# Optimization experiments

Hardware: AMD Instinct MI355X
Metric: run time of the kernel (lower is better)

Reference implementation:

```python
import jax, jax.numpy as jnp
import numpy as np

N_NODES = 50000
N_EDGES = 800000
H = 128          # hidden_channels
R = 20           # num_radial
L = 3            # num_layers
CUTOFF = 5.0
N_ATOM_TYPE = 100


def setup_inputs() -> dict:
    key = jax.random.key(0)
    ks = jax.random.split(key, 24)
    z = jax.random.randint(ks[0], (N_NODES,), 0, N_ATOM_TYPE)
    edge_index = jax.random.randint(ks[1], (2, N_EDGES), 0, N_NODES)
    # distances in (0.05, cutoff] so the 1/d term in the RBF stays bounded
    edge_dist = 0.05 + jax.random.uniform(ks[2], (N_EDGES,), jnp.float32) * (CUTOFF - 0.05)
    edge_vec = jax.random.normal(ks[3], (N_EDGES, 3), jnp.float32)
    s = 0.05
    emb = jax.random.normal(ks[4], (N_ATOM_TYPE, H), jnp.float32) * s
    # stacked per-layer params, torch Linear stored as [in, out]
    msg_w1 = jax.random.normal(ks[5], (L, H, H), jnp.float32) * s
    msg_b1 = jnp.zeros((L, H), jnp.float32)
    msg_w2 = jax.random.normal(ks[6], (L, H, 3 * H), jnp.float32) * s
    msg_b2 = jnp.zeros((L, 3 * H), jnp.float32)
    rbf_w = jax.random.normal(ks[7], (L, R, 3 * H), jnp.float32) * s
    rbf_b = jnp.zeros((L, 3 * H), jnp.float32)
    upd_vw = jax.random.normal(ks[8], (L, H, 2 * H), jnp.float32) * s
    upd_w1 = jax.random.normal(ks[9], (L, 2 * H, H), jnp.float32) * s
    upd_b1 = jnp.zeros((L, H), jnp.float32)
    upd_w2 = jax.random.normal(ks[10], (L, H, 3 * H), jnp.float32) * s
    upd_b2 = jnp.zeros((L, 3 * H), jnp.float32)
    out_w1 = jax.random.normal(ks[11], (H, H // 2), jnp.float32) * s
    out_b1 = jnp.zeros((H // 2,), jnp.float32)
    out_w2 = jax.random.normal(ks[12], (H // 2, 1), jnp.float32) * s
    out_b2 = jnp.zeros((1,), jnp.float32)
    return {
        "z": z, "edge_index": edge_index, "edge_dist": edge_dist, "edge_vec": edge_vec,
        "emb": emb,
        "msg_w1": msg_w1, "msg_b1": msg_b1, "msg_w2": msg_w2, "msg_b2": msg_b2,
        "rbf_w": rbf_w, "rbf_b": rbf_b,
        "upd_vw": upd_vw, "upd_w1": upd_w1, "upd_b1": upd_b1,
        "upd_w2": upd_w2, "upd_b2": upd_b2,
        "out_w1": out_w1, "out_b1": out_b1, "out_w2": out_w2, "out_b2": out_b2,
    }


def reference(z, edge_index, edge_dist, edge_vec, emb,
              msg_w1, msg_b1, msg_w2, msg_b2, rbf_w, rbf_b,
              upd_vw, upd_w1, upd_b1, upd_w2, upd_b2,
              out_w1, out_b1, out_w2, out_b2):
    inv_sqrt3 = 1.0 / float(np.sqrt(3.0))
    inv_sqrtH = 1.0 / float(np.sqrt(H))
    inv_sqrt2 = 1.0 / float(np.sqrt(2.0))

    src, dst = edge_index[0], edge_index[1]
    n_nodes = z.shape[0]

    # unit edge direction vectors
    unit = edge_vec / jnp.linalg.norm(edge_vec, axis=-1, keepdims=True)

    # radial basis (RadialBasisLayer)
    d = edge_dist[:, None]                                   # [E,1]
    cosc = 0.5 * (jnp.cos(jnp.pi * edge_dist / CUTOFF) + 1.0)
    cosc = jnp.where(edge_dist <= CUTOFF, cosc, 0.0)         # [E]
    n_idx = jnp.arange(1, R + 1, dtype=edge_dist.dtype)       # [R]
    rbf = (jnp.sin(n_idx * jnp.pi * d / CUTOFF) / d) * cosc[:, None]  # [E,R]

    s = emb[z]                                                # [N,H]
    v = jnp.zeros((n_nodes, 3, H), s.dtype)                   # [N,3,H]

    for l in range(L):
        # --- MessageBlock ---
        mf = jax.nn.silu(s @ msg_w1[l] + msg_b1[l]) @ msg_w2[l] + msg_b2[l]  # [N,3H]
        wf = rbf @ rbf_w[l] + rbf_b[l]                                       # [E,3H]
        prod = mf[src] * wf                                                  # [E,3H]
        w_s, w_vs, w_vv = jnp.split(prod, 3, axis=-1)                        # [E,H] x3
        w_v = v[src] * w_vs[:, None, :] * inv_sqrt3 + w_vv[:, None, :] * unit[:, :, None]  # [E,3,H]
        ds = jax.ops.segment_sum(w_s, dst, num_segments=n_nodes)             # [N,H]
        dv = jax.ops.segment_sum(w_v, dst, num_segments=n_nodes) * inv_sqrtH # [N,3,H]
        s = s + ds
        v = v + dv

        # --- UpdateBlock ---
        vv = v @ upd_vw[l]                                                   # [N,3,2H]
        v1, v2 = jnp.split(vv, 2, axis=-1)                                   # [N,3,H] x2
        v_dot = jnp.einsum('nij,nij->nj', v1, v2) * inv_sqrtH                # [N,H]
        v_norm = jnp.sqrt(jnp.sum(v2 * v2, axis=1) + 1e-12)                  # [N,H]
        feat = jnp.concatenate([s, v_norm], axis=-1)                         # [N,2H]
        uf = jax.nn.silu(feat @ upd_w1[l] + upd_b1[l]) @ upd_w2[l] + upd_b2[l]  # [N,3H]
        a_ss, a_sv, a_v = jnp.split(uf, 3, axis=-1)
        s = s + (v_dot * a_sv + a_ss) * inv_sqrt2
        v = v + v1 * a_v[:, None, :]

    # output MLP + mean readout
    h = jax.nn.silu(s @ out_w1 + out_b1) @ out_w2 + out_b2                   # [N,1]
    return jnp.mean(h, axis=0)                                               # [1]
```

## Files before the change

### kernel.cpp

```cpp
#include <hip/hip_runtime.h>
#include <hip/hip_bf16.h>
#include <math.h>

__device__ __forceinline__ float silu_f(float x) { return x / (1.0f + expf(-x)); }

__global__ __launch_bounds__(256) void k_init_s(const int* __restrict__ z,
                                                const float* __restrict__ emb,
                                                float* __restrict__ s, int total4) {
    int idx = blockIdx.x * 256 + threadIdx.x;
    if (idx < total4) {
        int n = idx >> 5, c4 = idx & 31;
        ((float4*)s)[idx] = ((const float4*)emb)[(size_t)z[n] * 32 + c4];
    }
}

__global__ __launch_bounds__(256) void k_count(const int* __restrict__ ei, int* __restrict__ cnt,
                                               int nE) {
    int e = blockIdx.x * 256 + threadIdx.x;
    if (e < nE) atomicAdd(&cnt[ei[nE + e]], 1);
}

__global__ __launch_bounds__(1024) void k_scan_blk(const int* __restrict__ cnt,
                                                   int* __restrict__ offs,
                                                   int* __restrict__ btot, int N) {
    __shared__ int tmp[1024];
    const int tid = threadIdx.x;
    int i = blockIdx.x * 1024 + tid;
    int val = (i < N) ? cnt[i] : 0;
    tmp[tid] = val;
    __syncthreads();
    for (int off = 1; off < 1024; off <<= 1) {
        int t = (tid >= off) ? tmp[tid - off] : 0;
        __syncthreads();
        tmp[tid] += t;
        __syncthreads();
    }
    if (i < N) offs[i] = tmp[tid] - val;
    if (tid == 1023) btot[blockIdx.x] = tmp[1023];
}

__global__ void k_scan_top(const int* __restrict__ btot, int* __restrict__ btot2,
                           int nb, int* __restrict__ offsN) {
    int tid = threadIdx.x;
    int v = (tid < nb) ? btot[tid] : 0;
    int orig = v;
    #pragma unroll
    for (int off = 1; off < 64; off <<= 1) {
        int u = __shfl_up(v, off, 64);
        if (tid >= off) v += u;
    }
    btot2[tid] = v - orig;
    if (tid == 63) *offsN = v;
}

__global__ __launch_bounds__(256) void k_scan_add(int* __restrict__ offs,
                                                  const int* __restrict__ btot2, int N) {
    int i = blockIdx.x * 256 + threadIdx.x;
    if (i < N) offs[i] += btot2[i >> 10];
}

__global__ __launch_bounds__(256) void k_fill(const int* __restrict__ ei,
                                              const int* __restrict__ offs,
                                              int* __restrict__ cur, int* __restrict__ perm,
                                              int nE) {
    int e = blockIdx.x * 256 + threadIdx.x;
    if (e < nE) {
        int d = ei[nE + e];
        int p = atomicAdd(&cur[d], 1);
        perm[offs[d] + p] = e;
    }
}

__global__ __launch_bounds__(256) void k_prep(const float* __restrict__ edist,
                                              int* __restrict__ perm,
                                              float2* __restrict__ curc2,
                                              int nE, int nEpad) {
    int i = blockIdx.x * 256 + threadIdx.x;
    if (i >= nEpad) return;
    if (i >= nE) { perm[i] = 0; curc2[i] = make_float2(0.f, 0.f); return; }
    int e = perm[i];
    float dd = edist[e];
    float t = 0.62831853071795864769f * dd;
    float cs = cosf(t), sn = sinf(t);
    float cosc = (dd <= 5.0f) ? (0.5f * (cs + 1.0f)) : 0.0f;
    float ic = cosc / dd;
    curc2[i] = make_float2(sn * ic, 2.0f * cs);
}

__global__ __launch_bounds__(256, 4) void k_mf(const float* __restrict__ s,
                                               const float* __restrict__ W1,
                                               const float* __restrict__ b1,
                                               const float* __restrict__ W2,
                                               const float* __restrict__ b2,
                                               float* __restrict__ mf) {
    __shared__ float s_t[16 * 128];
    __shared__ float h_t[16 * 128];
    const int tid = threadIdx.x;
    const size_t nb = (size_t)blockIdx.x * 16;
    {
        const float4* p = (const float4*)(s + nb * 128);
        ((float4*)s_t)[tid] = p[tid];
        ((float4*)s_t)[tid + 256] = p[tid + 256];
    }
    __syncthreads();
    const int c = tid & 127;
    const int g = tid >> 7;
    {
        float acc[8];
        float bb = b1[c];
        #pragma unroll
        for (int i = 0; i < 8; i++) acc[i] = bb;
        for (int k = 0; k < 128; k += 4) {
            float4 sv[8];
            #pragma unroll
            for (int i = 0; i < 8; i++) sv[i] = *(const float4*)&s_t[(g * 8 + i) * 128 + k];
            #pragma unroll
            for (int kk = 0; kk < 4; kk++) {
                float w = W1[(size_t)(k + kk) * 128 + c];
                #pragma unroll
                for (int i = 0; i < 8; i++) acc[i] = fmaf((&sv[i].x)[kk], w, acc[i]);
            }
        }
        #pragma unroll
        for (int i = 0; i < 8; i++) h_t[(g * 8 + i) * 128 + c] = silu_f(acc[i]);
    }
    __syncthreads();
    {
        float acc[8][3];
        #pragma unroll
        for (int q = 0; q < 3; q++) {
            float bb = b2[c + 128 * q];
            #pragma unroll
            for (int i = 0; i < 8; i++) acc[i][q] = bb;
        }
        for (int k = 0; k < 128; k += 4) {
            float4 hv[8];
            #pragma unroll
            for (int i = 0; i < 8; i++) hv[i] = *(const float4*)&h_t[(g * 8 + i) * 128 + k];
            #pragma unroll
            for (int kk = 0; kk < 4; kk++) {
                float w0 = W2[(size_t)(k + kk) * 384 + c];
                float w1 = W2[(size_t)(k + kk) * 384 + c + 128];
                float w2 = W2[(size_t)(k + kk) * 384 + c + 256];
                #pragma unroll
                for (int i = 0; i < 8; i++) {
                    float a = (&hv[i].x)[kk];
                    acc[i][0] = fmaf(a, w0, acc[i][0]);
                    acc[i][1] = fmaf(a, w1, acc[i][1]);
                    acc[i][2] = fmaf(a, w2, acc[i][2]);
                }
            }
        }
        #pragma unroll
        for (int i = 0; i < 8; i++)
            #pragma unroll
            for (int q = 0; q < 3; q++)
                mf[(nb + g * 8 + i) * 384 + c + 128 * q] = acc[i][q];
    }
}

__global__ __launch_bounds__(256, 2) void k_edge3(const int* __restrict__ ei,
                                                  const float* __restrict__ evec,
                                                  const float* __restrict__ mf,
                                                  const float* __restrict__ v,
                                                  const float* __restrict__ Wr,
                                                  const float* __restrict__ br,
                                                  const int* __restrict__ offs,
                                                  const int* __restrict__ perm,
                                                  const float2* __restrict__ curc2,
                                                  float* __restrict__ s,
                                                  float* __restrict__ dV,
                                                  int nN) {
    __shared__ float wrl[8064];
    for (int t = threadIdx.x; t < 8064; t += 256)
        wrl[t] = (t < 7680) ? Wr[t] : br[t - 7680];
    __syncthreads();

    const int lane = threadIdx.x & 63;
    const int wvi = __builtin_amdgcn_readfirstlane(threadIdx.x >> 6);
    const int nbase = blockIdx.x * 16 + wvi * 4;
    const float inv_sqrt3 = 0.57735026918962576451f;

    float brv[6];
    #pragma unroll
    for (int q = 0; q < 6; ++q) brv[q] = wrl[7680 + q * 64 + lane];

    for (int j = 0; j < 4; ++j) {
        const int n = nbase + j;
        if (n >= nN) break;
        const int beg = offs[n], end = offs[n + 1];

        float sa0 = 0.f, sa1 = 0.f;
        float dv00 = 0.f, dv10 = 0.f, dv20 = 0.f;
        float dv01 = 0.f, dv11 = 0.f, dv21 = 0.f;

        for (int i = beg; i < end; i += 4) {
            const int ne = end - i;
            int src[4];
            float ux[4], uy[4], uz[4], cur[4], prev[4], c2v[4];
            #pragma unroll
            for (int t = 0; t < 4; ++t) {
                int e = perm[i + t];
                float2 cc = curc2[i + t];
                cur[t] = cc.x; c2v[t] = cc.y; prev[t] = 0.f;
                src[t] = ei[e];
                float ex = evec[3 * e], ey = evec[3 * e + 1], ez = evec[3 * e + 2];
                float rn = 1.0f / sqrtf(ex * ex + ey * ey + ez * ez);
                ux[t] = ex * rn; uy[t] = ey * rn; uz[t] = ez * rn;
            }
            float wf[4][6];
            #pragma unroll
            for (int t = 0; t < 4; ++t)
                #pragma unroll
                for (int q = 0; q < 6; ++q) wf[t][q] = brv[q];
            for (int rr = 0; rr < 20; ++rr) {
                float w6[6];
                #pragma unroll
                for (int q = 0; q < 6; ++q) w6[q] = wrl[rr * 384 + q * 64 + lane];
                #pragma unroll
                for (int t = 0; t < 4; ++t) {
                    float c = cur[t];
                    #pragma unroll
                    for (int q = 0; q < 6; ++q) wf[t][q] = fmaf(c, w6[q], wf[t][q]);
                    float nx = fmaf(c2v[t], c, -prev[t]);
                    prev[t] = c; cur[t] = nx;
                }
            }
            #pragma unroll
            for (int t = 0; t < 4; ++t) {
                if (t < ne) {
                    const float* mfr = mf + (size_t)src[t] * 384 + lane;
                    const float* vr  = v  + (size_t)src[t] * 384 + lane;
                    sa0 = fmaf(wf[t][0], mfr[0],  sa0);
                    sa1 = fmaf(wf[t][1], mfr[64], sa1);
                    float a0 = wf[t][2] * mfr[128] * inv_sqrt3;
                    float a1 = wf[t][3] * mfr[192] * inv_sqrt3;
                    float b0 = wf[t][4] * mfr[256];
                    float b1 = wf[t][5] * mfr[320];
                    dv00 = fmaf(vr[0],   a0, fmaf(ux[t], b0, dv00));
                    dv10 = fmaf(vr[128], a0, fmaf(uy[t], b0, dv10));
                    dv20 = fmaf(vr[256], a0, fmaf(uz[t], b0, dv20));
                    dv01 = fmaf(vr[64],  a1, fmaf(ux[t], b1, dv01));
                    dv11 = fmaf(vr[192], a1, fmaf(uy[t], b1, dv11));
                    dv21 = fmaf(vr[320], a1, fmaf(uz[t], b1, dv21));
                }
            }
        }
        float* sp = s + (size_t)n * 128;
        sp[lane] += sa0;
        sp[64 + lane] += sa1;
        float* dp = dV + (size_t)n * 384;
        dp[lane] = dv00;        dp[64 + lane] = dv01;
        dp[128 + lane] = dv10;  dp[192 + lane] = dv11;
        dp[256 + lane] = dv20;  dp[320 + lane] = dv21;
    }
}

__global__ __launch_bounds__(256, 4) void k_upd(float* __restrict__ s,
                                                float* __restrict__ v,
                                                const float* __restrict__ dV,
                                                const float* __restrict__ Wv,
                                                const float* __restrict__ W1,
                                                const float* __restrict__ b1,
                                                const float* __restrict__ W2,
                                                const float* __restrict__ b2) {
    __shared__ float sv[8 * 128];
    __shared__ float vn[8 * 384];
    __shared__ float vnl[8 * 128];
    __shared__ float u1[8 * 128];
    const int tid = threadIdx.x;
    const size_t nb = (size_t)blockIdx.x * 8;
    const float inv_sqrtH = 0.08838834764831845f;
    const float inv_sqrt2 = 0.70710678118654752440f;

    {
        ((float4*)sv)[tid] = ((const float4*)(s + nb * 128))[tid];
        const float4* v4 = (const float4*)(v + nb * 384);
        const float4* e4 = (const float4*)(dV + nb * 384);
        #pragma unroll
        for (int t = 0; t < 3; ++t) {
            float4 av = v4[tid + 256 * t], bv = e4[tid + 256 * t];
            ((float4*)vn)[tid + 256 * t] =
                make_float4(fmaf(bv.x, inv_sqrtH, av.x), fmaf(bv.y, inv_sqrtH, av.y),
                            fmaf(bv.z, inv_sqrtH, av.z), fmaf(bv.w, inv_sqrtH, av.w));
        }
    }
    __syncthreads();
    const int c0 = tid & 63;
    const int ty = tid >> 6;
    float acc[2][3][4];
    {
        #pragma unroll
        for (int i = 0; i < 2; i++)
            #pragma unroll
            for (int d = 0; d < 3; d++)
                #pragma unroll
                for (int cc = 0; cc < 4; cc++) acc[i][d][cc] = 0.f;
        for (int k = 0; k < 128; k += 4) {
            float4 av[2][3];
            #pragma unroll
            for (int i = 0; i < 2; i++)
                #pragma unroll
                for (int d = 0; d < 3; d++)
                    av[i][d] = *(const float4*)&vn[(ty * 2 + i) * 384 + d * 128 + k];
            #pragma unroll
            for (int kk = 0; kk < 4; kk++) {
                float wc[4];
                #pragma unroll
                for (int cc = 0; cc < 4; cc++) wc[cc] = Wv[(size_t)(k + kk) * 256 + c0 + 64 * cc];
                #pragma unroll
                for (int i = 0; i < 2; i++)
                    #pragma unroll
                    for (int d = 0; d < 3; d++) {
                        float a = (&av[i][d].x)[kk];
                        #pragma unroll
                        for (int cc = 0; cc < 4; cc++)
                            acc[i][d][cc] = fmaf(a, wc[cc], acc[i][d][cc]);
                    }
            }
        }
    }
    float vdot[2][2];
    {
        #pragma unroll
        for (int i = 0; i < 2; i++)
            #pragma unroll
            for (int hh = 0; hh < 2; hh++) {
                float d0 = acc[i][0][hh] * acc[i][0][hh + 2] + acc[i][1][hh] * acc[i][1][hh + 2] +
                           acc[i][2][hh] * acc[i][2][hh + 2];
                vdot[i][hh] = d0 * inv_sqrtH;
                float n2 = acc[i][0][hh + 2] * acc[i][0][hh + 2] +
                           acc[i][1][hh + 2] * acc[i][1][hh + 2] +
                           acc[i][2][hh + 2] * acc[i][2][hh + 2];
                vnl[(ty * 2 + i) * 128 + c0 + 64 * hh] = sqrtf(n2 + 1e-12f);
            }
    }
    __syncthreads();
    {
        float a3[2][2];
        float bb0 = b1[c0], bb1 = b1[c0 + 64];
        #pragma unroll
        for (int i = 0; i < 2; i++) { a3[i][0] = bb0; a3[i][1] = bb1; }
        for (int k = 0; k < 128; k += 4) {
            float4 f[2];
            #pragma unroll
            for (int i = 0; i < 2; i++) f[i] = *(const float4*)&sv[(ty * 2 + i) * 128 + k];
            #pragma unroll
            for (int kk = 0; kk < 4; kk++) {
                float w0 = W1[(size_t)(k + kk) * 128 + c0];
                float w1 = W1[(size_t)(k + kk) * 128 + c0 + 64];
                #pragma unroll
                for (int i = 0; i < 2; i++) {
                    float a = (&f[i].x)[kk];
                    a3[i][0] = fmaf(a, w0, a3[i][0]);
                    a3[i][1] = fmaf(a, w1, a3[i][1]);
                }
            }
        }
        for (int k = 0; k < 128; k += 4) {
            float4 f[2];
            #pragma unroll
            for (int i = 0; i < 2; i++) f[i] = *(const float4*)&vnl[(ty * 2 + i) * 128 + k];
            #pragma unroll
            for (int kk = 0; kk < 4; kk++) {
                float w0 = W1[(size_t)(k + kk + 128) * 128 + c0];
                float w1 = W1[(size_t)(k + kk + 128) * 128 + c0 + 64];
                #pragma unroll
                for (int i = 0; i < 2; i++) {
                    float a = (&f[i].x)[kk];
                    a3[i][0] = fmaf(a, w0, a3[i][0]);
                    a3[i][1] = fmaf(a, w1, a3[i][1]);
                }
            }
        }
        #pragma unroll
        for (int i = 0; i < 2; i++) {
            u1[(ty * 2 + i) * 128 + c0] = silu_f(a3[i][0]);
            u1[(ty * 2 + i) * 128 + c0 + 64] = silu_f(a3[i][1]);
        }
    }
    __syncthreads();
    {
        float a4[2][6];
        #pragma unroll
        for (int q = 0; q < 6; q++) {
            float bb = b2[c0 + 64 * q];
            #pragma unroll
            for (int i = 0; i < 2; i++) a4[i][q] = bb;
        }
        for (int k = 0; k < 128; k += 4) {
            float4 uu[2];
            #pragma unroll
            for (int i = 0; i < 2; i++) uu[i] = *(const float4*)&u1[(ty * 2 + i) * 128 + k];
            #pragma unroll
            for (int kk = 0; kk < 4; kk++) {
                float w[6];
                #pragma unroll
                for (int q = 0; q < 6; q++) w[q] = W2[(size_t)(k + kk) * 384 + c0 + 64 * q];
                #pragma unroll
                for (int i = 0; i < 2; i++) {
                    float a = (&uu[i].x)[kk];
                    #pragma unroll
                    for (int q = 0; q < 6; q++) a4[i][q] = fmaf(a, w[q], a4[i][q]);
                }
            }
        }
        #pragma unroll
        for (int i = 0; i < 2; i++) {
            int node = ty * 2 + i;
            size_t nr = nb + node;
            #pragma unroll
            for (int hh = 0; hh < 2; ++hh) {
                int h = c0 + 64 * hh;
                float a_ss = a4[i][hh], a_sv = a4[i][2 + hh], a_v = a4[i][4 + hh];
                s[nr * 128 + h] = sv[node * 128 + h] + (vdot[i][hh] * a_sv + a_ss) * inv_sqrt2;
                #pragma unroll
                for (int d = 0; d < 3; ++d)
                    v[nr * 384 + d * 128 + h] =
                        vn[node * 384 + d * 128 + h] + acc[i][d][hh] * a_v;
            }
        }
    }
}

__global__ __launch_bounds__(256, 4) void k_out(const float* __restrict__ s,
                                                const float* __restrict__ ow1,
                                                const float* __restrict__ ob1,
                                                const float* __restrict__ ow2,
                                                const float* __restrict__ ob2,
                                                float* __restrict__ out, int nNodes) {
    __shared__ float st[16 * 128];
    __shared__ float red[4];
    const int tid = threadIdx.x;
    const size_t nb = (size_t)blockIdx.x * 16;
    {
        const float4* p = (const float4*)(s + nb * 128);
        ((float4*)st)[tid] = p[tid];
        ((float4*)st)[tid + 256] = p[tid + 256];
    }
    __syncthreads();
    const int c = tid & 63;
    const int ty = tid >> 6;
    float acc[4];
    float bb = ob1[c];
    #pragma unroll
    for (int i = 0; i < 4; i++) acc[i] = bb;
    for (int k = 0; k < 128; k += 4) {
        float4 sv[4];
        #pragma unroll
        for (int i = 0; i < 4; i++) sv[i] = *(const float4*)&st[(ty * 4 + i) * 128 + k];
        #pragma unroll
        for (int kk = 0; kk < 4; kk++) {
            float w = ow1[(size_t)(k + kk) * 64 + c];
            #pragma unroll
            for (int i = 0; i < 4; i++) acc[i] = fmaf((&sv[i].x)[kk], w, acc[i]);
        }
    }
    float w2 = ow2[c];
    float p = 0.f;
    #pragma unroll
    for (int i = 0; i < 4; i++) p += silu_f(acc[i]) * w2;
    #pragma unroll
    for (int off = 32; off > 0; off >>= 1) p += __shfl_down(p, off, 64);
    if (c == 0) red[ty] = p;
    __syncthreads();
    if (tid == 0) {
        float val = (red[0] + red[1] + red[2] + red[3]) * (1.0f / (float)nNodes);
        if (blockIdx.x == 0) val += ob2[0];
        atomicAdd(out, val);
    }
}

extern "C" void kernel_launch(void* const* d_in, const int* in_sizes, int n_in,
                              void* d_out, int out_size, void* d_ws, size_t ws_size,
                              hipStream_t stream) {
    const int*   z     = (const int*)d_in[0];
    const int*   ei    = (const int*)d_in[1];
    const float* edist = (const float*)d_in[2];
    const float* evec  = (const float*)d_in[3];
    const float* emb   = (const float*)d_in[4];
    const float* mw1   = (const float*)d_in[5];
    const float* mb1   = (const float*)d_in[6];
    const float* mw2   = (const float*)d_in[7];
    const float* mb2   = (const float*)d_in[8];
    const float* rw    = (const float*)d_in[9];
    const float* rbb   = (const float*)d_in[10];
    const float* uvw   = (const float*)d_in[11];
    const float* uw1   = (const float*)d_in[12];
    const float* ub1   = (const float*)d_in[13];
    const float* uw2   = (const float*)d_in[14];
    const float* ub2   = (const float*)d_in[15];
    const float* ow1   = (const float*)d_in[16];
    const float* ob1   = (const float*)d_in[17];
    const float* ow2   = (const float*)d_in[18];
    const float* ob2   = (const float*)d_in[19];

    const int N = in_sizes[0];
    const int E = in_sizes[2];
    const int Ep = E + 4;

    const size_t need = ((size_t)N * 1280 + (N + 1) + Ep) * 4 + (size_t)Ep * 8;
    hipMemsetAsync(d_out, 0, out_size * sizeof(float), stream);
    if (ws_size < need) return;

    float* ws = (float*)d_ws;
    float*  s     = ws;
    float*  v     = s + (size_t)N * 128;
    float*  mf    = v + (size_t)N * 384;
    float*  dV    = mf + (size_t)N * 384;
    int*    offs  = (int*)(dV + (size_t)N * 384);
    int*    perm  = offs + (N + 1);
    float2* curc2 = (float2*)(perm + Ep);
    int*    cnt   = (int*)curc2;
    int*    cur   = cnt + N;
    int*    btot  = cur + N;
    int*    btot2 = btot + 64;

    hipMemsetAsync(v, 0, (size_t)N * 384 * sizeof(float), stream);
    hipMemsetAsync(cnt, 0, (size_t)2 * N * sizeof(int), stream);

    const int nbScan = (N + 1023) / 1024;
    k_count<<<(E + 255) / 256, 256, 0, stream>>>(ei, cnt, E);
    k_scan_blk<<<nbScan, 1024, 0, stream>>>(cnt, offs, btot, N);
    k_scan_top<<<1, 64, 0, stream>>>(btot, btot2, nbScan, offs + N);
    k_scan_add<<<(N + 255) / 256, 256, 0, stream>>>(offs, btot2, N);
    k_fill<<<(E + 255) / 256, 256, 0, stream>>>(ei, offs, cur, perm, E);
    k_prep<<<(Ep + 255) / 256, 256, 0, stream>>>(edist, perm, curc2, E, Ep);

    k_init_s<<<(N * 32 + 255) / 256, 256, 0, stream>>>(z, emb, s, N * 32);

    for (int l = 0; l < 3; ++l) {
        k_mf<<<N / 16, 256, 0, stream>>>(s, mw1 + (size_t)l * 16384, mb1 + l * 128,
                                         mw2 + (size_t)l * 49152, mb2 + l * 384, mf);
        k_edge3<<<(N + 15) / 16, 256, 0, stream>>>(ei, evec, mf, v,
                                                   rw + (size_t)l * 7680, rbb + l * 384,
                                                   offs, perm, curc2, s, dV, N);
        k_upd<<<N / 8, 256, 0, stream>>>(s, v, dV, uvw + (size_t)l * 32768,
                                         uw1 + (size_t)l * 32768, ub1 + l * 128,
                                         uw2 + (size_t)l * 49152, ub2 + l * 384);
    }
    k_out<<<N / 16, 256, 0, stream>>>(s, ow1, ob1, ow2, ob2, (float*)d_out, N);
}
```

Baseline: 3.193 ms.

## Software-pipeline edge gathers and double node tile in update kernel

The edge kernel now double-buffers per-edge metadata (perm, source index, unit vector, Chebyshev state) using A/B register sets. It also issues the mf and v gathers for the current group of four edges before the radial-basis FMA loop, so gather latency overlaps with compute. The update kernel processes 16 nodes per block instead of 8, which doubles reuse of each weight load from global memory, and its occupancy hint drops from 4 to 3. The costs are much higher register pressure in both kernels, possible spills, and lower occupancy. The padded perm/curc2 arrays are assumed to cover the prefetch tail.

Result: slower. 9.546 ms (+199.0%).

```diff
diff --git a/kernel.cpp b/kernel.cpp
--- a/kernel.cpp
+++ b/kernel.cpp
@@ -159,7 +159,68 @@
     }
 }
 
-__global__ __launch_bounds__(256, 2) void k_edge3(const int* __restrict__ ei,
+#define LOAD_META(SUF, II)                                                     \
+    _Pragma("unroll")                                                          \
+    for (int t = 0; t < 4; ++t) {                                              \
+        int e = perm[(II) + t];                                                \
+        float2 cc = curc2[(II) + t];                                           \
+        cur##SUF[t] = cc.x; c2##SUF[t] = cc.y; prev##SUF[t] = 0.f;             \
+        src##SUF[t] = ei[e];                                                   \
+        float ex = evec[3 * e], ey = evec[3 * e + 1], ez = evec[3 * e + 2];    \
+        float rn = 1.0f / sqrtf(ex * ex + ey * ey + ez * ez);                  \
+        ux##SUF[t] = ex * rn; uy##SUF[t] = ey * rn; uz##SUF[t] = ez * rn;      \
+    }
+
+#define PROC(CUR, OTH)                                                         \
+    {                                                                          \
+        float gm[4][6], gv[4][6];                                              \
+        _Pragma("unroll")                                                      \
+        for (int t = 0; t < 4; ++t) {                                          \
+            const float* mfr = mf + (size_t)src##CUR[t] * 384 + lane;          \
+            const float* vr  = v  + (size_t)src##CUR[t] * 384 + lane;          \
+            _Pragma("unroll")                                                  \
+            for (int q = 0; q < 6; ++q) { gm[t][q] = mfr[q * 64]; gv[t][q] = vr[q * 64]; } \
+        }                                                                      \
+        if (i + 4 < end) { LOAD_META(OTH, i + 4) }                             \
+        float wf[4][6];                                                        \
+        _Pragma("unroll")                                                      \
+        for (int t = 0; t < 4; ++t)                                            \
+            _Pragma("unroll")                                                  \
+            for (int q = 0; q < 6; ++q) wf[t][q] = brv[q];                     \
+        for (int rr = 0; rr < 20; ++rr) {                                      \
+            float w6[6];                                                       \
+            _Pragma("unroll")                                                  \
+            for (int q = 0; q < 6; ++q) w6[q] = wrl[rr * 384 + q * 64 + lane]; \
+            _Pragma("unroll")                                                  \
+            for (int t = 0; t < 4; ++t) {                                      \
+                float c = cur##CUR[t];                                         \
+                _Pragma("unroll")                                              \
+                for (int q = 0; q < 6; ++q) wf[t][q] = fmaf(c, w6[q], wf[t][q]); \
+                float nx = fmaf(c2##CUR[t], c, -prev##CUR[t]);                 \
+                prev##CUR[t] = c; cur##CUR[t] = nx;                            \
+            }                                                                  \
+        }                                                                      \
+        const int ne = end - i;                                                \
+        _Pragma("unroll")                                                      \
+        for (int t = 0; t < 4; ++t) {                                          \
+            if (t < ne) {                                                      \
+                sa0 = fmaf(wf[t][0], gm[t][0], sa0);                           \
+                sa1 = fmaf(wf[t][1], gm[t][1], sa1);                           \
+                float a0 = wf[t][2] * gm[t][2] * inv_sqrt3;                    \
+                float a1 = wf[t][3] * gm[t][3] * inv_sqrt3;                    \
+                float b0 = wf[t][4] * gm[t][4];                                \
+                float b1 = wf[t][5] * gm[t][5];                                \
+                dv00 = fmaf(gv[t][0], a0, fmaf(ux##CUR[t], b0, dv00));         \
+                dv10 = fmaf(gv[t][2], a0, fmaf(uy##CUR[t], b0, dv10));         \
+                dv20 = fmaf(gv[t][4], a0, fmaf(uz##CUR[t], b0, dv20));         \
+                dv01 = fmaf(gv[t][1], a1, fmaf(ux##CUR[t], b1, dv01));         \
+                dv11 = fmaf(gv[t][3], a1, fmaf(uy##CUR[t], b1, dv11));         \
+                dv21 = fmaf(gv[t][5], a1, fmaf(uz##CUR[t], b1, dv21));         \
+            }                                                                  \
+        }                                                                      \
+    }
+
+__global__ __launch_bounds__(256, 2) void k_edge4(const int* __restrict__ ei,
                                                   const float* __restrict__ evec,
                                                   const float* __restrict__ mf,
                                                   const float* __restrict__ v,
@@ -194,58 +255,20 @@
         float dv00 = 0.f, dv10 = 0.f, dv20 = 0.f;
         float dv01 = 0.f, dv11 = 0.f, dv21 = 0.f;
 
-        for (int i = beg; i < end; i += 4) {
-            const int ne = end - i;
-            int src[4];
-            float ux[4], uy[4], uz[4], cur[4], prev[4], c2v[4];
-            #pragma unroll
-            for (int t = 0; t < 4; ++t) {
-                int e = perm[i + t];
-                float2 cc = curc2[i + t];
-                cur[t] = cc.x; c2v[t] = cc.y; prev[t] = 0.f;
-                src[t] = ei[e];
-                float ex = evec[3 * e], ey = evec[3 * e + 1], ez = evec[3 * e + 2];
-                float rn = 1.0f / sqrtf(ex * ex + ey * ey + ez * ez);
-                ux[t] = ex * rn; uy[t] = ey * rn; uz[t] = ez * rn;
-            }
-            float wf[4][6];
-            #pragma unroll
-            for (int t = 0; t < 4; ++t)
-                #pragma unroll
-                for (int q = 0; q < 6; ++q) wf[t][q] = brv[q];
-            for (int rr = 0; rr < 20; ++rr) {
-                float w6[6];
-                #pragma unroll
-                for (int q = 0; q < 6; ++q) w6[q] = wrl[rr * 384 + q * 64 + lane];
-                #pragma unroll
-                for (int t = 0; t < 4; ++t) {
-                    float c = cur[t];
-                    #pragma unroll
-                    for (int q = 0; q < 6; ++q) wf[t][q] = fmaf(c, w6[q], wf[t][q]);
-                    float nx = fmaf(c2v[t], c, -prev[t]);
-                    prev[t] = c; cur[t] = nx;
-                }
-            }
-            #pragma unroll
-            for (int t = 0; t < 4; ++t) {
-                if (t < ne) {
-                    const float* mfr = mf + (size_t)src[t] * 384 + lane;
-                    const float* vr  = v  + (size_t)src[t] * 384 + lane;
-                    sa0 = fmaf(wf[t][0], mfr[0],  sa0);
-                    sa1 = fmaf(wf[t][1], mfr[64], sa1);
-                    float a0 = wf[t][2] * mfr[128] * inv_sqrt3;
-                    float a1 = wf[t][3] * mfr[192] * inv_sqrt3;
-                    float b0 = wf[t][4] * mfr[256];
-                    float b1 = wf[t][5] * mfr[320];
-                    dv00 = fmaf(vr[0],   a0, fmaf(ux[t], b0, dv00));
-                    dv10 = fmaf(vr[128], a0, fmaf(uy[t], b0, dv10));
-                    dv20 = fmaf(vr[256], a0, fmaf(uz[t], b0, dv20));
-                    dv01 = fmaf(vr[64],  a1, fmaf(ux[t], b1, dv01));
-                    dv11 = fmaf(vr[192], a1, fmaf(uy[t], b1, dv11));
-                    dv21 = fmaf(vr[320], a1, fmaf(uz[t], b1, dv21));
-                }
-            }
-        }
+        int srcA[4], srcB[4];
+        float uxA[4], uyA[4], uzA[4], curA[4], prevA[4], c2A[4];
+        float uxB[4], uyB[4], uzB[4], curB[4], prevB[4], c2B[4];
+
+        int i = beg;
+        if (i < end) { LOAD_META(A, i) }
+        while (i < end) {
+            PROC(A, B)
+            i += 4;
+            if (i >= end) break;
+            PROC(B, A)
+            i += 4;
+        }
+
         float* sp = s + (size_t)n * 128;
         sp[lane] += sa0;
         sp[64 + lane] += sa1;
@@ -256,7 +279,7 @@
     }
 }
 
-__global__ __launch_bounds__(256, 4) void k_upd(float* __restrict__ s,
+__global__ __launch_bounds__(256, 3) void k_upd(float* __restrict__ s,
                                                 float* __restrict__ v,
                                                 const float* __restrict__ dV,
                                                 const float* __restrict__ Wv,
@@ -264,21 +287,23 @@
                                                 const float* __restrict__ b1,
                                                 const float* __restrict__ W2,
                                                 const float* __restrict__ b2) {
-    __shared__ float sv[8 * 128];
-    __shared__ float vn[8 * 384];
-    __shared__ float vnl[8 * 128];
-    __shared__ float u1[8 * 128];
+    __shared__ float sv[16 * 128];
+    __shared__ float vn[16 * 384];
+    __shared__ float vnl[16 * 128];
+    __shared__ float u1[16 * 128];
     const int tid = threadIdx.x;
-    const size_t nb = (size_t)blockIdx.x * 8;
+    const size_t nb = (size_t)blockIdx.x * 16;
     const float inv_sqrtH = 0.08838834764831845f;
     const float inv_sqrt2 = 0.70710678118654752440f;
 
     {
-        ((float4*)sv)[tid] = ((const float4*)(s + nb * 128))[tid];
+        const float4* s4 = (const float4*)(s + nb * 128);
+        ((float4*)sv)[tid] = s4[tid];
+        ((float4*)sv)[tid + 256] = s4[tid + 256];
         const float4* v4 = (const float4*)(v + nb * 384);
         const float4* e4 = (const float4*)(dV + nb * 384);
         #pragma unroll
-        for (int t = 0; t < 3; ++t) {
+        for (int t = 0; t < 6; ++t) {
             float4 av = v4[tid + 256 * t], bv = e4[tid + 256 * t];
             ((float4*)vn)[tid + 256 * t] =
                 make_float4(fmaf(bv.x, inv_sqrtH, av.x), fmaf(bv.y, inv_sqrtH, av.y),
@@ -288,28 +313,28 @@
     __syncthreads();
     const int c0 = tid & 63;
     const int ty = tid >> 6;
-    float acc[2][3][4];
-    {
-        #pragma unroll
-        for (int i = 0; i < 2; i++)
+    float acc[4][3][4];
+    {
+        #pragma unroll
+        for (int i = 0; i < 4; i++)
             #pragma unroll
             for (int d = 0; d < 3; d++)
                 #pragma unroll
                 for (int cc = 0; cc < 4; cc++) acc[i][d][cc] = 0.f;
         for (int k = 0; k < 128; k += 4) {
-            float4 av[2][3];
-            #pragma unroll
-            for (int i = 0; i < 2; i++)
+            float4 av[4][3];
+            #pragma unroll
+            for (int i = 0; i < 4; i++)
                 #pragma unroll
                 for (int d = 0; d < 3; d++)
-                    av[i][d] = *(const float4*)&vn[(ty * 2 + i) * 384 + d * 128 + k];
+                    av[i][d] = *(const float4*)&vn[(ty * 4 + i) * 384 + d * 128 + k];
             #pragma unroll
             for (int kk = 0; kk < 4; kk++) {
                 float wc[4];
                 #pragma unroll
                 for (int cc = 0; cc < 4; cc++) wc[cc] = Wv[(size_t)(k + kk) * 256 + c0 + 64 * cc];
                 #pragma unroll
-                for (int i = 0; i < 2; i++)
+                for (int i = 0; i < 4; i++)
                     #pragma unroll
                     for (int d = 0; d < 3; d++) {
                         float a = (&av[i][d].x)[kk];
@@ -320,10 +345,10 @@
             }
         }
     }
-    float vdot[2][2];
-    {
-        #pragma unroll
-        for (int i = 0; i < 2; i++)
+    float vdot[4][2];
+    {
+        #pragma unroll
+        for (int i = 0; i < 4; i++)
             #pragma unroll
             for (int hh = 0; hh < 2; hh++) {
                 float d0 = acc[i][0][hh] * acc[i][0][hh + 2] + acc[i][1][hh] * acc[i][1][hh + 2] +
@@ -332,25 +357,25 @@
                 float n2 = acc[i][0][hh + 2] * acc[i][0][hh + 2] +
                            acc[i][1][hh + 2] * acc[i][1][hh + 2] +
                            acc[i][2][hh + 2] * acc[i][2][hh + 2];
-                vnl[(ty * 2 + i) * 128 + c0 + 64 * hh] = sqrtf(n2 + 1e-12f);
-            }
-    }
-    __syncthreads();
-    {
-        float a3[2][2];
+                vnl[(ty * 4 + i) * 128 + c0 + 64 * hh] = sqrtf(n2 + 1e-12f);
+            }
+    }
+    __syncthreads();
+    {
+        float a3[4][2];
         float bb0 = b1[c0], bb1 = b1[c0 + 64];
         #pragma unroll
-        for (int i = 0; i < 2; i++) { a3[i][0] = bb0; a3[i][1] = bb1; }
+        for (int i = 0; i < 4; i++) { a3[i][0] = bb0; a3[i][1] = bb1; }
         for (int k = 0; k < 128; k += 4) {
-            float4 f[2];
-            #pragma unroll
-            for (int i = 0; i < 2; i++) f[i] = *(const float4*)&sv[(ty * 2 + i) * 128 + k];
+            float4 f[4];
+            #pragma unroll
+            for (int i = 0; i < 4; i++) f[i] = *(const float4*)&sv[(ty * 4 + i) * 128 + k];
             #pragma unroll
             for (int kk = 0; kk < 4; kk++) {
                 float w0 = W1[(size_t)(k + kk) * 128 + c0];
                 float w1 = W1[(size_t)(k + kk) * 128 + c0 + 64];
                 #pragma unroll
-                for (int i = 0; i < 2; i++) {
+                for (int i = 0; i < 4; i++) {
                     float a = (&f[i].x)[kk];
                     a3[i][0] = fmaf(a, w0, a3[i][0]);
                     a3[i][1] = fmaf(a, w1, a3[i][1]);
@@ -358,15 +383,15 @@
             }
         }
         for (int k = 0; k < 128; k += 4) {
-            float4 f[2];
-            #pragma unroll
-            for (int i = 0; i < 2; i++) f[i] = *(const float4*)&vnl[(ty * 2 + i) * 128 + k];
+            float4 f[4];
+            #pragma unroll
+            for (int i = 0; i < 4; i++) f[i] = *(const float4*)&vnl[(ty * 4 + i) * 128 + k];
             #pragma unroll
             for (int kk = 0; kk < 4; kk++) {
                 float w0 = W1[(size_t)(k + kk + 128) * 128 + c0];
                 float w1 = W1[(size_t)(k + kk + 128) * 128 + c0 + 64];
                 #pragma unroll
-                for (int i = 0; i < 2; i++) {
+                for (int i = 0; i < 4; i++) {
                     float a = (&f[i].x)[kk];
                     a3[i][0] = fmaf(a, w0, a3[i][0]);
                     a3[i][1] = fmaf(a, w1, a3[i][1]);
@@ -374,31 +399,31 @@
             }
         }
         #pragma unroll
-        for (int i = 0; i < 2; i++) {
-            u1[(ty * 2 + i) * 128 + c0] = silu_f(a3[i][0]);
-            u1[(ty * 2 + i) * 128 + c0 + 64] = silu_f(a3[i][1]);
-        }
-    }
-    __syncthreads();
-    {
-        float a4[2][6];
+        for (int i = 0; i < 4; i++) {
+            u1[(ty * 4 + i) * 128 + c0] = silu_f(a3[i][0]);
+            u1[(ty * 4 + i) * 128 + c0 + 64] = silu_f(a3[i][1]);
+        }
+    }
+    __syncthreads();
+    {
+        float a4[4][6];
         #pragma unroll
         for (int q = 0; q < 6; q++) {
             float bb = b2[c0 + 64 * q];
             #pragma unroll
-            for (int i = 0; i < 2; i++) a4[i][q] = bb;
+            for (int i = 0; i < 4; i++) a4[i][q] = bb;
         }
         for (int k = 0; k < 128; k += 4) {
-            float4 uu[2];
-            #pragma unroll
-            for (int i = 0; i < 2; i++) uu[i] = *(const float4*)&u1[(ty * 2 + i) * 128 + k];
+            float4 uu[4];
+            #pragma unroll
+            for (int i = 0; i < 4; i++) uu[i] = *(const float4*)&u1[(ty * 4 + i) * 128 + k];
             #pragma unroll
             for (int kk = 0; kk < 4; kk++) {
                 float w[6];
                 #pragma unroll
                 for (int q = 0; q < 6; q++) w[q] = W2[(size_t)(k + kk) * 384 + c0 + 64 * q];
                 #pragma unroll
-                for (int i = 0; i < 2; i++) {
+                for (int i = 0; i < 4; i++) {
                     float a = (&uu[i].x)[kk];
                     #pragma unroll
                     for (int q = 0; q < 6; q++) a4[i][q] = fmaf(a, w[q], a4[i][q]);
@@ -406,8 +431,8 @@
             }
         }
         #pragma unroll
-        for (int i = 0; i < 2; i++) {
-            int node = ty * 2 + i;
+        for (int i = 0; i < 4; i++) {
+            int node = ty * 4 + i;
             size_t nr = nb + node;
             #pragma unroll
             for (int hh = 0; hh < 2; ++hh) {
@@ -532,12 +557,12 @@
     for (int l = 0; l < 3; ++l) {
         k_mf<<<N / 16, 256, 0, stream>>>(s, mw1 + (size_t)l * 16384, mb1 + l * 128,
                                          mw2 + (size_t)l * 49152, mb2 + l * 384, mf);
-        k_edge3<<<(N + 15) / 16, 256, 0, stream>>>(ei, evec, mf, v,
+        k_edge4<<<(N + 15) / 16, 256, 0, stream>>>(ei, evec, mf, v,
                                                    rw + (size_t)l * 7680, rbb + l * 384,
                                                    offs, perm, curc2, s, dV, N);
-        k_upd<<<N / 8, 256, 0, stream>>>(s, v, dV, uvw + (size_t)l * 32768,
-                                         uw1 + (size_t)l * 32768, ub1 + l * 128,
-                                         uw2 + (size_t)l * 49152, ub2 + l * 384);
+        k_upd<<<N / 16, 256, 0, stream>>>(s, v, dV, uvw + (size_t)l * 32768,
+                                          uw1 + (size_t)l * 32768, ub1 + l * 128,
+                                          uw2 + (size_t)l * 49152, ub2 + l * 384);
     }
     k_out<<<N / 16, 256, 0, stream>>>(s, ow1, ob1, ow2, ob2, (float*)d_out, N);
 }
```
